# Kernel optimization log

Hardware: AMD Instinct MI355X
Metric: run time of the kernel (lower is better)

Reference implementation:

```python
import jax, jax.numpy as jnp
import numpy as np

N = 100000
E = 1600000

def _build_adj(edge_index):
    # add self-loops (set_diag), then symmetric DAD normalization
    loops = jnp.arange(N, dtype=edge_index.dtype)
    row = jnp.concatenate([edge_index[0], loops])
    col = jnp.concatenate([edge_index[1], loops])
    deg = jax.ops.segment_sum(jnp.ones_like(row, dtype=jnp.float32), row, num_segments=N)
    dinv = jnp.where(deg > 0, jax.lax.rsqrt(deg), 0.0)
    norm = dinv[row] * dinv[col]  # [E+N]
    return row, col, norm

def _spmm(row, col, norm, h):
    # out[row] += norm * h[col]  (A_hat @ h)
    return jax.ops.segment_sum(norm[:, None] * h[col], row, num_segments=N)

def setup_inputs() -> dict:
    key = jax.random.key(0)
    ks = jax.random.split(key, 8)
    nfeat, nhid, nclass = 128, 128, 64
    s = lambda d: (1.0 / np.sqrt(d)).astype(np.float32)
    return {
        "x": jax.random.normal(ks[0], (N, nfeat), jnp.float32),
        "edge_index": jax.random.randint(ks[1], (2, E), 0, N, dtype=jnp.int64),
        "W0": jax.random.normal(ks[2], (nfeat, nhid), jnp.float32) * s(nfeat),
        "b0": jnp.zeros((nhid,), jnp.float32),
        "W1": jax.random.normal(ks[3], (nhid, nhid), jnp.float32) * s(nhid),
        "b1": jnp.zeros((nhid,), jnp.float32),
        "W2": jax.random.normal(ks[4], (nhid, nclass), jnp.float32) * s(nhid),
        "b2": jnp.zeros((nclass,), jnp.float32),
    }

def reference(x, edge_index, W0, b0, W1, b1, W2, b2):
    row, col, norm = _build_adj(edge_index)
    # layer 1: GCNConv + relu (dropout inactive in eval mode)
    h = jax.nn.relu(_spmm(row, col, norm, x @ W0) + b0)
    # layer 2
    h = jax.nn.relu(_spmm(row, col, norm, h @ W1) + b1)
    # final layer, no activation
    return _spmm(row, col, norm, h @ W2) + b2
```

## Files before the change

kernel.cpp:

```cpp
#include <hip/hip_runtime.h>
#include <hip/hip_bf16.h>

#define NN 100000
#define NE 1600000
#define BK 98
#define CAP 18432
#define CHUNK 8192

typedef _Float16 f16;
typedef f16 f16x8 __attribute__((ext_vector_type(8)));
typedef float f32x4 __attribute__((ext_vector_type(4)));


__global__ void zero_i32(int* __restrict__ p, int n) {
    int i = blockIdx.x * blockDim.x + threadIdx.x;
    if (i < n) p[i] = 0;
}

__global__ __launch_bounds__(256) void bin_edges(const int* __restrict__ row,
                                                 const int* __restrict__ col,
                                                 int* __restrict__ bcursor,
                                                 int2* __restrict__ binned) {
    __shared__ int  bcnt[BK];
    __shared__ int  bbase[BK];
    __shared__ int  lstart[BK + 1];
    __shared__ int  bcur[BK];
    __shared__ int2 stage[CHUNK];
    int tid = threadIdx.x;
    int e0 = blockIdx.x * CHUNK;
    int emax = min(CHUNK, NE - e0);

    if (tid < BK) bcnt[tid] = 0;
    __syncthreads();
    for (int i = tid; i < emax; i += 256)
        atomicAdd(&bcnt[row[e0 + i] >> 10], 1);
    __syncthreads();
    if (tid == 0) {
        int s = 0;
        for (int b = 0; b < BK; ++b) { lstart[b] = s; s += bcnt[b]; }
        lstart[BK] = s;
    }
    __syncthreads();
    if (tid < BK) {
        bcur[tid]  = lstart[tid];
        bbase[tid] = atomicAdd(&bcursor[tid], bcnt[tid]);
    }
    __syncthreads();
    for (int i = tid; i < emax; i += 256) {
        int r = row[e0 + i], c = col[e0 + i];
        int pos = atomicAdd(&bcur[r >> 10], 1);
        stage[pos] = make_int2(r, c);
    }
    __syncthreads();
    for (int i = tid; i < emax; i += 256) {
        int2 rc = stage[i];
        int b = rc.x >> 10;
        binned[(size_t)b * CAP + bbase[b] + (i - lstart[b])] = rc;
    }
}

__global__ __launch_bounds__(1024) void build_csr(const int* __restrict__ bcount,
                                                  const int2* __restrict__ binned,
                                                  int* __restrict__ offsets,
                                                  float* __restrict__ dinv,
                                                  int* __restrict__ csr_col) {
    __shared__ int cnt[1024];
    __shared__ int sc[1024];
    __shared__ int colbuf[CAP];
    __shared__ int mybase_s;
    int tid = threadIdx.x;
    int b = blockIdx.x;
    int r0 = b << 10;
    int nrows = min(1024, NN - r0);

    if (tid < BK) sc[tid] = bcount[tid];
    cnt[tid] = 0;
    __syncthreads();
    if (tid == 0) {
        int s = 0;
        for (int i = 0; i < b; ++i) s += sc[i];
        mybase_s = s;
    }
    int n = sc[b];
    __syncthreads();
    int mybase = mybase_s;
    const int2* src = binned + (size_t)b * CAP;

    for (int i = tid; i < n; i += 1024)
        atomicAdd(&cnt[src[i].x - r0], 1);
    __syncthreads();

    int v = cnt[tid];
    sc[tid] = v;
    __syncthreads();
    #pragma unroll
    for (int s = 1; s < 1024; s <<= 1) {
        int t = (tid >= s) ? sc[tid - s] : 0;
        __syncthreads();
        sc[tid] += t;
        __syncthreads();
    }
    int incl = sc[tid];
    if (tid < nrows) {
        offsets[r0 + tid + 1] = mybase + incl;
        dinv[r0 + tid] = rsqrtf((float)(v + 1));
    }
    if (b == 0 && tid == 0) offsets[0] = 0;

    cnt[tid] = incl - v;
    __syncthreads();
    for (int i = tid; i < n; i += 1024) {
        int2 rc = src[i];
        int pos = atomicAdd(&cnt[rc.x - r0], 1);
        colbuf[pos] = rc.y;
    }
    __syncthreads();
    for (int i = tid; i < n; i += 1024)
        csr_col[mybase + i] = colbuf[i];
}

template<int F, bool AFP32>
__global__ __launch_bounds__(256) void gemm_mfma(const void* __restrict__ Ain,
                                                 const float* __restrict__ W,
                                                 const float* __restrict__ dinv,
                                                 f16* __restrict__ T) {
    constexpr int PITCH = 136;
    __shared__ f16 Wt[F * PITCH];
    int tid = threadIdx.x;
    for (int e = tid; e < 128 * F; e += 256) {
        int k = e / F, n = e - k * F;
        Wt[n * PITCH + k] = (f16)W[e];
    }
    __syncthreads();

    int wave = tid >> 6;
    int lane = tid & 63;
    int m = lane & 15, q = lane >> 4;
    int r0 = blockIdx.x * 64 + wave * 16;
    int ra = min(r0 + m, NN - 1);

    constexpr int NT = F / 16;
    f32x4 acc[NT];
    #pragma unroll
    for (int t = 0; t < NT; ++t) acc[t] = (f32x4){0.f, 0.f, 0.f, 0.f};

    #pragma unroll
    for (int c = 0; c < 4; ++c) {
        f16x8 a;
        if (AFP32) {
            const float* Af = (const float*)Ain;
            const float4* p = (const float4*)&Af[(size_t)ra * 128 + c * 32 + q * 8];
            float4 lo = p[0], hi = p[1];
            a[0] = (f16)lo.x; a[1] = (f16)lo.y; a[2] = (f16)lo.z; a[3] = (f16)lo.w;
            a[4] = (f16)hi.x; a[5] = (f16)hi.y; a[6] = (f16)hi.z; a[7] = (f16)hi.w;
        } else {
            const f16* Ah = (const f16*)Ain;
            a = *(const f16x8*)&Ah[(size_t)ra * 128 + c * 32 + q * 8];
        }
        #pragma unroll
        for (int t = 0; t < NT; ++t) {
            f16x8 b = *(const f16x8*)&Wt[(t * 16 + m) * PITCH + c * 32 + q * 8];
            acc[t] = __builtin_amdgcn_mfma_f32_16x16x32_f16(a, b, acc[t], 0, 0, 0);
        }
    }

    int rows[4];
    float dv[4];
    #pragma unroll
    for (int i = 0; i < 4; ++i) {
        rows[i] = r0 + q * 4 + i;
        dv[i] = dinv[min(rows[i], NN - 1)];
    }
    #pragma unroll
    for (int t = 0; t < NT; ++t) {
        #pragma unroll
        for (int i = 0; i < 4; ++i) {
            if (rows[i] < NN) {
                T[(size_t)rows[i] * F + t * 16 + m] = (f16)(acc[t][i] * dv[i]);
            }
        }
    }
}

template<int F, bool RELU, bool OUTF16>
__global__ __launch_bounds__(256) void spmm_h(const f16* __restrict__ T,
                                              const int* __restrict__ offsets,
                                              const int* __restrict__ csr_col,
                                              const float* __restrict__ dinv,
                                              const float* __restrict__ bias,
                                              void* __restrict__ outv) {
    constexpr int LPR = F / 8;
    constexpr int RPB = 256 / LPR;
    int lane = threadIdx.x % LPR;
    int rs   = threadIdx.x / LPR;
    int r    = blockIdx.x * RPB + rs;
    if (r >= NN) return;

    const f16x8* Tv = (const f16x8*)T;
    int o0 = offsets[r], o1 = offsets[r + 1];

    float s0[8], s1[8], s2[8], s3[8];
    f16x8 self = Tv[(size_t)r * LPR + lane];
    #pragma unroll
    for (int u = 0; u < 8; ++u) { s0[u] = (float)self[u]; s1[u] = 0.f; s2[u] = 0.f; s3[u] = 0.f; }

    int j = o0;
    for (; j + 4 <= o1; j += 4) {
        int c0 = csr_col[j], c1 = csr_col[j + 1], c2 = csr_col[j + 2], c3 = csr_col[j + 3];
        f16x8 v0 = Tv[(size_t)c0 * LPR + lane];
        f16x8 v1 = Tv[(size_t)c1 * LPR + lane];
        f16x8 v2 = Tv[(size_t)c2 * LPR + lane];
        f16x8 v3 = Tv[(size_t)c3 * LPR + lane];
        #pragma unroll
        for (int u = 0; u < 8; ++u) {
            s0[u] += (float)v0[u]; s1[u] += (float)v1[u];
            s2[u] += (float)v2[u]; s3[u] += (float)v3[u];
        }
    }
    for (; j < o1; ++j) {
        int c = csr_col[j];
        f16x8 v = Tv[(size_t)c * LPR + lane];
        #pragma unroll
        for (int u = 0; u < 8; ++u) s0[u] += (float)v[u];
    }

    float dr = dinv[r];
    float o[8];
    #pragma unroll
    for (int u = 0; u < 8; ++u) {
        float s = (s0[u] + s1[u]) + (s2[u] + s3[u]);
        o[u] = fmaf(dr, s, bias[lane * 8 + u]);
        if (RELU) o[u] = fmaxf(o[u], 0.f);
    }

    if (OUTF16) {
        f16x8 h;
        #pragma unroll
        for (int u = 0; u < 8; ++u) h[u] = (f16)o[u];
        ((f16x8*)outv)[(size_t)r * LPR + lane] = h;
    } else {
        float* outF = (float*)outv;
        float4 lo = make_float4(o[0], o[1], o[2], o[3]);
        float4 hi = make_float4(o[4], o[5], o[6], o[7]);
        *(float4*)&outF[(size_t)r * F + lane * 8]     = lo;
        *(float4*)&outF[(size_t)r * F + lane * 8 + 4] = hi;
    }
}


extern "C" void kernel_launch(void* const* d_in, const int* in_sizes, int n_in,
                              void* d_out, int out_size, void* d_ws, size_t ws_size,
                              hipStream_t stream) {
    const float* x  = (const float*)d_in[0];
    const int*   ei = (const int*)d_in[1];
    const float* W0 = (const float*)d_in[2];
    const float* b0 = (const float*)d_in[3];
    const float* W1 = (const float*)d_in[4];
    const float* b1 = (const float*)d_in[5];
    const float* W2 = (const float*)d_in[6];
    const float* b2 = (const float*)d_in[7];
    float* out = (float*)d_out;

    const int* row = ei;
    const int* col = ei + NE;

    char* wsp = (char*)d_ws;
    auto alloc = [&](size_t bytes) {
        char* p = wsp;
        wsp += (bytes + 255) & ~(size_t)255;
        return p;
    };
    int*   bcursor = (int*)alloc((size_t)BK * 4);
    int2*  binned  = (int2*)alloc((size_t)BK * CAP * 8);
    int*   offsets = (int*)alloc((size_t)(NN + 1) * 4);
    float* dinv    = (float*)alloc((size_t)NN * 4);
    int*   csr_col = (int*)alloc((size_t)NE * 4);
    f16*   Tbuf    = (f16*)alloc((size_t)NN * 128 * 2);
    f16*   Hbuf    = (f16*)alloc((size_t)NN * 128 * 2);

    zero_i32<<<1, 256, 0, stream>>>(bcursor, BK);
    bin_edges<<<(NE + CHUNK - 1) / CHUNK, 256, 0, stream>>>(row, col, bcursor, binned);
    build_csr<<<BK, 1024, 0, stream>>>(bcursor, binned, offsets, dinv, csr_col);

    const int GB = (NN + 63) / 64;

    gemm_mfma<128, true><<<GB, 256, 0, stream>>>(x, W0, dinv, Tbuf);
    spmm_h<128, true, true><<<(NN + 15) / 16, 256, 0, stream>>>(Tbuf, offsets, csr_col, dinv, b0, Hbuf);
    gemm_mfma<128, false><<<GB, 256, 0, stream>>>(Hbuf, W1, dinv, Tbuf);
    spmm_h<128, true, true><<<(NN + 15) / 16, 256, 0, stream>>>(Tbuf, offsets, csr_col, dinv, b1, Hbuf);
    gemm_mfma<64, false><<<GB, 256, 0, stream>>>(Hbuf, W2, dinv, Tbuf);
    spmm_h<64, false, false><<<(NN + 31) / 32, 256, 0, stream>>>(Tbuf, offsets, csr_col, dinv, b2, out);
}
```

Before: 355.6 us.

## Store intermediate features in column-chunked layout and split SpMM by feature chunk

Intermediate feature matrices are stored as 16-column chunks laid out contiguously across all nodes, instead of row-major. SpMM blocks now each handle one 16-feature chunk for 128 rows, so each gather touches a 3.2 MB chunk that fits better in cache. GEMM reads and writes are updated to match the new layout. The cost is that each edge's column index and offsets are re-read once per chunk, and each gather is only 32 bytes per row.

```diff
diff --git a/kernel.cpp b/kernel.cpp
--- a/kernel.cpp
+++ b/kernel.cpp
@@ -147,7 +147,7 @@
     #pragma unroll
     for (int c = 0; c < 4; ++c) {
         f16x8 a;
-        if (AFP32) {
+        if constexpr (AFP32) {
             const float* Af = (const float*)Ain;
             const float4* p = (const float4*)&Af[(size_t)ra * 128 + c * 32 + q * 8];
             float4 lo = p[0], hi = p[1];
@@ -155,7 +155,8 @@
             a[4] = (f16)hi.x; a[5] = (f16)hi.y; a[6] = (f16)hi.z; a[7] = (f16)hi.w;
         } else {
             const f16* Ah = (const f16*)Ain;
-            a = *(const f16x8*)&Ah[(size_t)ra * 128 + c * 32 + q * 8];
+            int kc = 2 * c + (q >> 1);
+            a = *(const f16x8*)&Ah[((size_t)kc * NN + ra) * 16 + (q & 1) * 8];
         }
         #pragma unroll
         for (int t = 0; t < NT; ++t) {
@@ -176,7 +177,7 @@
         #pragma unroll
         for (int i = 0; i < 4; ++i) {
             if (rows[i] < NN) {
-                T[(size_t)rows[i] * F + t * 16 + m] = (f16)(acc[t][i] * dv[i]);
+                T[((size_t)t * NN + rows[i]) * 16 + m] = (f16)(acc[t][i] * dv[i]);
             }
         }
     }
@@ -189,28 +190,29 @@
                                               const float* __restrict__ dinv,
                                               const float* __restrict__ bias,
                                               void* __restrict__ outv) {
-    constexpr int LPR = F / 8;
-    constexpr int RPB = 256 / LPR;
-    int lane = threadIdx.x % LPR;
-    int rs   = threadIdx.x / LPR;
-    int r    = blockIdx.x * RPB + rs;
+    constexpr int NCH = F / 16;
+    int c  = blockIdx.x % NCH;
+    int rb = blockIdx.x / NCH;
+    int lane = threadIdx.x & 1;
+    int rs   = threadIdx.x >> 1;
+    int r    = rb * 128 + rs;
     if (r >= NN) return;
 
-    const f16x8* Tv = (const f16x8*)T;
+    const f16x8* Tv = (const f16x8*)(T + (size_t)c * NN * 16);
     int o0 = offsets[r], o1 = offsets[r + 1];
 
     float s0[8], s1[8], s2[8], s3[8];
-    f16x8 self = Tv[(size_t)r * LPR + lane];
+    f16x8 self = Tv[(size_t)r * 2 + lane];
     #pragma unroll
     for (int u = 0; u < 8; ++u) { s0[u] = (float)self[u]; s1[u] = 0.f; s2[u] = 0.f; s3[u] = 0.f; }
 
     int j = o0;
     for (; j + 4 <= o1; j += 4) {
         int c0 = csr_col[j], c1 = csr_col[j + 1], c2 = csr_col[j + 2], c3 = csr_col[j + 3];
-        f16x8 v0 = Tv[(size_t)c0 * LPR + lane];
-        f16x8 v1 = Tv[(size_t)c1 * LPR + lane];
-        f16x8 v2 = Tv[(size_t)c2 * LPR + lane];
-        f16x8 v3 = Tv[(size_t)c3 * LPR + lane];
+        f16x8 v0 = Tv[(size_t)c0 * 2 + lane];
+        f16x8 v1 = Tv[(size_t)c1 * 2 + lane];
+        f16x8 v2 = Tv[(size_t)c2 * 2 + lane];
+        f16x8 v3 = Tv[(size_t)c3 * 2 + lane];
         #pragma unroll
         for (int u = 0; u < 8; ++u) {
             s0[u] += (float)v0[u]; s1[u] += (float)v1[u];
@@ -218,8 +220,8 @@
         }
     }
     for (; j < o1; ++j) {
-        int c = csr_col[j];
-        f16x8 v = Tv[(size_t)c * LPR + lane];
+        int cc = csr_col[j];
+        f16x8 v = Tv[(size_t)cc * 2 + lane];
         #pragma unroll
         for (int u = 0; u < 8; ++u) s0[u] += (float)v[u];
     }
@@ -229,7 +231,7 @@
     #pragma unroll
     for (int u = 0; u < 8; ++u) {
         float s = (s0[u] + s1[u]) + (s2[u] + s3[u]);
-        o[u] = fmaf(dr, s, bias[lane * 8 + u]);
+        o[u] = fmaf(dr, s, bias[c * 16 + lane * 8 + u]);
         if (RELU) o[u] = fmaxf(o[u], 0.f);
     }
 
@@ -237,13 +239,13 @@
         f16x8 h;
         #pragma unroll
         for (int u = 0; u < 8; ++u) h[u] = (f16)o[u];
-        ((f16x8*)outv)[(size_t)r * LPR + lane] = h;
+        ((f16x8*)outv)[((size_t)c * NN + r) * 2 + lane] = h;
     } else {
         float* outF = (float*)outv;
         float4 lo = make_float4(o[0], o[1], o[2], o[3]);
         float4 hi = make_float4(o[4], o[5], o[6], o[7]);
-        *(float4*)&outF[(size_t)r * F + lane * 8]     = lo;
-        *(float4*)&outF[(size_t)r * F + lane * 8 + 4] = hi;
+        *(float4*)&outF[(size_t)r * F + c * 16 + lane * 8]     = lo;
+        *(float4*)&outF[(size_t)r * F + c * 16 + lane * 8 + 4] = hi;
     }
 }
 
@@ -283,11 +285,12 @@
     build_csr<<<BK, 1024, 0, stream>>>(bcursor, binned, offsets, dinv, csr_col);
 
     const int GB = (NN + 63) / 64;
+    const int RB = (NN + 127) / 128;
 
     gemm_mfma<128, true><<<GB, 256, 0, stream>>>(x, W0, dinv, Tbuf);
-    spmm_h<128, true, true><<<(NN + 15) / 16, 256, 0, stream>>>(Tbuf, offsets, csr_col, dinv, b0, Hbuf);
+    spmm_h<128, true, true><<<8 * RB, 256, 0, stream>>>(Tbuf, offsets, csr_col, dinv, b0, Hbuf);
     gemm_mfma<128, false><<<GB, 256, 0, stream>>>(Hbuf, W1, dinv, Tbuf);
-    spmm_h<128, true, true><<<(NN + 15) / 16, 256, 0, stream>>>(Tbuf, offsets, csr_col, dinv, b1, Hbuf);
+    spmm_h<128, true, true><<<8 * RB, 256, 0, stream>>>(Tbuf, offsets, csr_col, dinv, b1, Hbuf);
     gemm_mfma<64, false><<<GB, 256, 0, stream>>>(Hbuf, W2, dinv, Tbuf);
-    spmm_h<64, false, false><<<(NN + 31) / 32, 256, 0, stream>>>(Tbuf, offsets, csr_col, dinv, b2, out);
-}
+    spmm_h<64, false, false><<<4 * RB, 256, 0, stream>>>(Tbuf, offsets, csr_col, dinv, b2, out);
+}
```

Result: slower. 417.6 us (+17.4%).

## Fuse SpMM aggregation with the following layer GEMM in one kernel

Applied to the files above, without the earlier changes.

Adds a spmm_gemm kernel in which each block gathers and sums 32 rows of neighbor features, applies bias, ReLU and normalization, keeps the result in shared memory, and multiplies it by the next layer's weights with MFMA before writing the transformed rows. This replaces the separate spmm and gemm launches for layers 1 and 2, which removes the round trip of the hidden activations through global memory and two kernel launches. The zeroing kernel is also swapped for hipMemsetAsync. In exchange each block converts the full weight matrix into LDS, and 512-thread blocks with heavier register use may lower occupancy for the gather phase.

```diff
diff --git a/kernel.cpp b/kernel.cpp
--- a/kernel.cpp
+++ b/kernel.cpp
@@ -11,11 +11,6 @@
 typedef f16 f16x8 __attribute__((ext_vector_type(8)));
 typedef float f32x4 __attribute__((ext_vector_type(4)));
 
-
-__global__ void zero_i32(int* __restrict__ p, int n) {
-    int i = blockIdx.x * blockDim.x + threadIdx.x;
-    if (i < n) p[i] = 0;
-}
 
 __global__ __launch_bounds__(256) void bin_edges(const int* __restrict__ row,
                                                  const int* __restrict__ col,
@@ -147,7 +142,7 @@
     #pragma unroll
     for (int c = 0; c < 4; ++c) {
         f16x8 a;
-        if (AFP32) {
+        if constexpr (AFP32) {
             const float* Af = (const float*)Ain;
             const float4* p = (const float4*)&Af[(size_t)ra * 128 + c * 32 + q * 8];
             float4 lo = p[0], hi = p[1];
@@ -179,6 +174,107 @@
                 T[(size_t)rows[i] * F + t * 16 + m] = (f16)(acc[t][i] * dv[i]);
             }
         }
+    }
+}
+
+template<int F2>
+__global__ __launch_bounds__(512, 6) void spmm_gemm(const f16* __restrict__ T,
+                                                    const int* __restrict__ offsets,
+                                                    const int* __restrict__ csr_col,
+                                                    const float* __restrict__ dinv,
+                                                    const float* __restrict__ bias,
+                                                    const float* __restrict__ W,
+                                                    f16* __restrict__ Tout) {
+    constexpr int PITCH = 136;
+    __shared__ f16 Wt[F2 * PITCH];
+    __shared__ f16 hbuf[32 * PITCH];
+    int tid = threadIdx.x;
+
+    for (int e = tid; e < 128 * F2; e += 512) {
+        int k = e / F2, n = e - k * F2;
+        Wt[n * PITCH + k] = (f16)W[e];
+    }
+
+    int lane = tid & 15;
+    int rs   = tid >> 4;
+    int r    = blockIdx.x * 32 + rs;
+
+    const f16x8* Tv = (const f16x8*)T;
+    int o0 = offsets[r], o1 = offsets[r + 1];
+
+    float s0[8], s1[8], s2[8], s3[8];
+    f16x8 self = Tv[(size_t)r * 16 + lane];
+    #pragma unroll
+    for (int u = 0; u < 8; ++u) { s0[u] = (float)self[u]; s1[u] = 0.f; s2[u] = 0.f; s3[u] = 0.f; }
+
+    int j = o0;
+    for (; j + 4 <= o1; j += 4) {
+        int c0 = csr_col[j], c1 = csr_col[j + 1], c2 = csr_col[j + 2], c3 = csr_col[j + 3];
+        f16x8 v0 = Tv[(size_t)c0 * 16 + lane];
+        f16x8 v1 = Tv[(size_t)c1 * 16 + lane];
+        f16x8 v2 = Tv[(size_t)c2 * 16 + lane];
+        f16x8 v3 = Tv[(size_t)c3 * 16 + lane];
+        #pragma unroll
+        for (int u = 0; u < 8; ++u) {
+            s0[u] += (float)v0[u]; s1[u] += (float)v1[u];
+            s2[u] += (float)v2[u]; s3[u] += (float)v3[u];
+        }
+    }
+    for (; j < o1; ++j) {
+        int c = csr_col[j];
+        f16x8 v = Tv[(size_t)c * 16 + lane];
+        #pragma unroll
+        for (int u = 0; u < 8; ++u) s0[u] += (float)v[u];
+    }
+
+    float dr = dinv[r];
+    f16x8 h;
+    #pragma unroll
+    for (int u = 0; u < 8; ++u) {
+        float s = (s0[u] + s1[u]) + (s2[u] + s3[u]);
+        float o = fmaf(dr, s, bias[lane * 8 + u]);
+        h[u] = (f16)fmaxf(o, 0.f);
+    }
+    *(f16x8*)&hbuf[rs * PITCH + lane * 8] = h;
+    __syncthreads();
+
+    int wv = tid >> 6, wl = tid & 63;
+    int m = wl & 15, q = wl >> 4;
+    constexpr int FW  = F2 / 4;
+    constexpr int NTW = FW / 16;
+    int rg = wv >> 2;
+    int fg = wv & 3;
+
+    f32x4 acc[NTW];
+    #pragma unroll
+    for (int t = 0; t < NTW; ++t) acc[t] = (f32x4){0.f, 0.f, 0.f, 0.f};
+
+    #pragma unroll
+    for (int c = 0; c < 4; ++c) {
+        f16x8 a = *(const f16x8*)&hbuf[(rg * 16 + m) * PITCH + c * 32 + q * 8];
+        #pragma unroll
+        for (int t = 0; t < NTW; ++t) {
+            f16x8 b = *(const f16x8*)&Wt[(fg * FW + t * 16 + m) * PITCH + c * 32 + q * 8];
+            acc[t] = __builtin_amdgcn_mfma_f32_16x16x32_f16(a, b, acc[t], 0, 0, 0);
+        }
+    }
+    __syncthreads();
+
+    #pragma unroll
+    for (int i = 0; i < 4; ++i) {
+        int rloc = rg * 16 + q * 4 + i;
+        float dv = dinv[blockIdx.x * 32 + rloc];
+        #pragma unroll
+        for (int t = 0; t < NTW; ++t)
+            hbuf[rloc * PITCH + fg * FW + t * 16 + m] = (f16)(acc[t][i] * dv);
+    }
+    __syncthreads();
+
+    constexpr int LPO = F2 / 8;
+    for (int e = tid; e < 32 * LPO; e += 512) {
+        int rr = e / LPO, ff = e - rr * LPO;
+        ((f16x8*)Tout)[(size_t)(blockIdx.x * 32 + rr) * LPO + ff] =
+            *(f16x8*)&hbuf[rr * PITCH + ff * 8];
     }
 }
 
@@ -278,16 +374,15 @@
     f16*   Tbuf    = (f16*)alloc((size_t)NN * 128 * 2);
     f16*   Hbuf    = (f16*)alloc((size_t)NN * 128 * 2);
 
-    zero_i32<<<1, 256, 0, stream>>>(bcursor, BK);
+    hipMemsetAsync(bcursor, 0, (size_t)BK * 4, stream);
     bin_edges<<<(NE + CHUNK - 1) / CHUNK, 256, 0, stream>>>(row, col, bcursor, binned);
     build_csr<<<BK, 1024, 0, stream>>>(bcursor, binned, offsets, dinv, csr_col);
 
     const int GB = (NN + 63) / 64;
+    const int FB = NN / 32;
 
     gemm_mfma<128, true><<<GB, 256, 0, stream>>>(x, W0, dinv, Tbuf);
-    spmm_h<128, true, true><<<(NN + 15) / 16, 256, 0, stream>>>(Tbuf, offsets, csr_col, dinv, b0, Hbuf);
-    gemm_mfma<128, false><<<GB, 256, 0, stream>>>(Hbuf, W1, dinv, Tbuf);
-    spmm_h<128, true, true><<<(NN + 15) / 16, 256, 0, stream>>>(Tbuf, offsets, csr_col, dinv, b1, Hbuf);
-    gemm_mfma<64, false><<<GB, 256, 0, stream>>>(Hbuf, W2, dinv, Tbuf);
+    spmm_gemm<128><<<FB, 512, 0, stream>>>(Tbuf, offsets, csr_col, dinv, b0, W1, Hbuf);
+    spmm_gemm<64><<<FB, 512, 0, stream>>>(Hbuf, offsets, csr_col, dinv, b1, W2, Tbuf);
     spmm_h<64, false, false><<<(NN + 31) / 32, 256, 0, stream>>>(Tbuf, offsets, csr_col, dinv, b2, out);
 }
```

Result: faster. 346.4 us (-2.6%).
